# Optimization experiments

Hardware: AMD Instinct MI355X
Metric: run time of the kernel (lower is better)

The kernel has to match this reference:

```python
import jax, jax.numpy as jnp
import numpy as np

N_HEADS = 16
N_KV_HEADS = 4
HEAD_DIM = 128


def _rope(x, cos, sin):
    # x: [b, s, h, d]; cos/sin: [s, d//2]; interleaved pair rotation
    b, s, h, d = x.shape
    xp = x.reshape(b, s, h, d // 2, 2)
    x_r, x_i = xp[..., 0], xp[..., 1]
    c = cos[None, :, None, :]
    sn = sin[None, :, None, :]
    o_r = x_r * c - x_i * sn
    o_i = x_r * sn + x_i * c
    return jnp.stack([o_r, o_i], axis=-1).reshape(b, s, h, d)


def setup_inputs() -> dict:
    key = jax.random.key(0)
    ks = jax.random.split(key, 7)
    B, S, D = 2, 2048, 2048
    KV = N_KV_HEADS * HEAD_DIM
    x = jax.random.normal(ks[0], (B, S, D), dtype=jnp.float32)
    freqs_cos = jax.random.uniform(ks[1], (S, HEAD_DIM // 2), dtype=jnp.float32)
    freqs_sin = jax.random.uniform(ks[2], (S, HEAD_DIM // 2), dtype=jnp.float32)
    scale = 0.02
    wq = jax.random.normal(ks[3], (D, D), dtype=jnp.float32) * scale
    wk = jax.random.normal(ks[4], (KV, D), dtype=jnp.float32) * scale
    wv = jax.random.normal(ks[5], (KV, D), dtype=jnp.float32) * scale
    wo = jax.random.normal(ks[6], (D, D), dtype=jnp.float32) * scale
    return {"x": x, "freqs_cos": freqs_cos, "freqs_sin": freqs_sin,
            "wq": wq, "wk": wk, "wv": wv, "wo": wo}


def reference(x, freqs_cos, freqs_sin, wq, wk, wv, wo):
    B, S, D = x.shape
    n_rep = N_HEADS // N_KV_HEADS
    q = (x @ wq.T).reshape(B, S, N_HEADS, HEAD_DIM)
    k = (x @ wk.T).reshape(B, S, N_KV_HEADS, HEAD_DIM)
    v = (x @ wv.T).reshape(B, S, N_KV_HEADS, HEAD_DIM)
    q = _rope(q, freqs_cos, freqs_sin)
    k = _rope(k, freqs_cos, freqs_sin)
    # repeat_kv == torch.repeat_interleave along head dim
    k = jnp.repeat(k, n_rep, axis=2)
    v = jnp.repeat(v, n_rep, axis=2)
    q = q.transpose(0, 2, 1, 3)  # [B, H, S, d]
    k = k.transpose(0, 2, 1, 3)
    v = v.transpose(0, 2, 1, 3)
    scale = 1.0 / np.sqrt(HEAD_DIM).astype(np.float32)
    scores = jnp.einsum('bhqd,bhkd->bhqk', q, k) * scale
    causal = jnp.tril(jnp.ones((S, S), dtype=bool))
    scores = jnp.where(causal[None, None], scores, jnp.finfo(jnp.float32).min)
    probs = jax.nn.softmax(scores.astype(jnp.float32), axis=-1).astype(q.dtype)
    out = jnp.einsum('bhqk,bhkd->bhqd', probs, v)
    out = out.transpose(0, 2, 1, 3).reshape(B, S, N_HEADS * HEAD_DIM)
    return out @ wo.T
```

## Files before the change

### kernel.cpp

```cpp
#include <hip/hip_runtime.h>
#include <hip/hip_bf16.h>
#include <type_traits>

using bf16x8 = __attribute__((ext_vector_type(8))) short;
using f32x4  = __attribute__((ext_vector_type(4))) float;
using u16x8  = __attribute__((ext_vector_type(8))) unsigned short;
using u16x4  = __attribute__((ext_vector_type(4))) unsigned short;
using u32x4  = __attribute__((ext_vector_type(4))) unsigned int;

__device__ __forceinline__ float b2f(unsigned short u) {
    unsigned int x = ((unsigned int)u) << 16;
    return __builtin_bit_cast(float, x);
}
__device__ __forceinline__ unsigned short f2b(float f) {
    __hip_bfloat16 h = __float2bfloat16(f);
    return __builtin_bit_cast(unsigned short, h);
}

#if defined(__has_builtin)
#if __has_builtin(__builtin_amdgcn_exp2f)
#define EXP2F(x) __builtin_amdgcn_exp2f(x)
#else
#define EXP2F(x) exp2f(x)
#endif
#else
#define EXP2F(x) exp2f(x)
#endif

__device__ __forceinline__ void async_copy16(const void* g, void* l) {
    __builtin_amdgcn_global_load_lds(
        (const __attribute__((address_space(1))) unsigned int*)g,
        (__attribute__((address_space(3))) unsigned int*)l, 16, 0, 0);
}

#define MFMA16(a, b, c) __builtin_amdgcn_mfma_f32_16x16x32_bf16(a, b, c, 0, 0, 0)

#define BARRIER() do { asm volatile("" ::: "memory"); \
    __builtin_amdgcn_s_barrier(); asm volatile("" ::: "memory"); } while (0)
#define VMCNT6() asm volatile("s_waitcnt vmcnt(6)" ::: "memory")
#define VMCNT0() asm volatile("s_waitcnt vmcnt(0)" ::: "memory")

__global__ __launch_bounds__(256) void cvt_f32_to_bf16(
    const float* __restrict__ s, unsigned short* __restrict__ d, int n4)
{
    int i = blockIdx.x * blockDim.x + threadIdx.x;
    if (i >= n4) return;
    float4 v = ((const float4*)s)[i];
    ushort4 o;
    o.x = f2b(v.x); o.y = f2b(v.y); o.z = f2b(v.z); o.w = f2b(v.w);
    ((ushort4*)d)[i] = o;
}

__global__ __launch_bounds__(512, 2) void qkv_gemm(
    const unsigned short* __restrict__ A,
    const unsigned short* __restrict__ Wq,
    const unsigned short* __restrict__ Wk,
    const unsigned short* __restrict__ Wv,
    unsigned short* __restrict__ Q,
    unsigned short* __restrict__ Kk,
    unsigned short* __restrict__ V)
{
    const int K = 2048;
    __shared__ unsigned short ldsA[2][256 * 64];
    __shared__ unsigned short ldsB[2][256 * 64];

    int tid  = threadIdx.x;
    int w    = tid >> 6;
    int lane = tid & 63;
    int idx  = lane & 15;
    int quad = lane >> 4;
    int srow   = lane >> 3;
    int schunk = (lane & 7) ^ srow;

    int wfm = (w >> 2) * 64;
    int wfn = (w & 3) * 64;

    int bid = (blockIdx.x & 7) * 24 + (blockIdx.x >> 3);
    int bm = bid / 12;
    int bn = bid - bm * 12;
    int m0 = bm * 256;

    const unsigned short* Bt;
    unsigned short* C;
    int Nc, n0;
    if (bn < 8)       { Bt = Wq + (size_t)bn * 256 * K;        C = Q;  Nc = 2048; n0 = bn * 256; }
    else if (bn < 10) { Bt = Wk + (size_t)(bn - 8) * 256 * K;  C = Kk; Nc = 512;  n0 = (bn - 8) * 256; }
    else              { Bt = Wv + (size_t)(bn - 10) * 256 * K; C = V;  Nc = 512;  n0 = (bn - 10) * 256; }

    const unsigned short* Ab = A + (size_t)m0 * K;

    f32x4 acc[8][4];
    #pragma unroll
    for (int mf = 0; mf < 8; ++mf)
        #pragma unroll
        for (int nf = 0; nf < 4; ++nf) acc[mf][nf] = (f32x4){0.f, 0.f, 0.f, 0.f};

    bf16x8 a[4][2], b0[2][2], b1[2][2];

    auto STAGE = [&](const unsigned short* __restrict__ G, int rb, int kc,
                     unsigned short* dst) {
        #pragma unroll
        for (int i = 0; i < 2; ++i) {
            int R = (w * 2 + i) * 8;
            async_copy16(G + (size_t)(rb + R + srow) * K + kc + schunk * 8,
                         dst + (size_t)R * 64);
        }
    };
    auto LDA = [&](int d, int mh) {
        #pragma unroll
        for (int mi = 0; mi < 4; ++mi) {
            int r = mh * 128 + wfm + mi * 16 + idx;
            #pragma unroll
            for (int ks = 0; ks < 2; ++ks)
                a[mi][ks] = *(const bf16x8*)&ldsA[d][r * 64 + (((ks * 4 + quad) ^ (r & 7)) << 3)];
        }
    };
    auto LDB0 = [&](int d, int nh) {
        #pragma unroll
        for (int nj = 0; nj < 2; ++nj) {
            int r = wfn + nh * 32 + nj * 16 + idx;
            #pragma unroll
            for (int ks = 0; ks < 2; ++ks)
                b0[nj][ks] = *(const bf16x8*)&ldsB[d][r * 64 + (((ks * 4 + quad) ^ (r & 7)) << 3)];
        }
    };
    auto LDB1 = [&](int d, int nh) {
        #pragma unroll
        for (int nj = 0; nj < 2; ++nj) {
            int r = wfn + nh * 32 + nj * 16 + idx;
            #pragma unroll
            for (int ks = 0; ks < 2; ++ks)
                b1[nj][ks] = *(const bf16x8*)&ldsB[d][r * 64 + (((ks * 4 + quad) ^ (r & 7)) << 3)];
        }
    };
    auto MM0 = [&](int mh, int nh) {
        __builtin_amdgcn_s_setprio(1);
        #pragma unroll
        for (int mi = 0; mi < 4; ++mi)
            #pragma unroll
            for (int nj = 0; nj < 2; ++nj)
                #pragma unroll
                for (int ks = 0; ks < 2; ++ks)
                    acc[mh * 4 + mi][nh * 2 + nj] =
                        MFMA16(a[mi][ks], b0[nj][ks], acc[mh * 4 + mi][nh * 2 + nj]);
        __builtin_amdgcn_s_setprio(0);
    };
    auto MM1 = [&](int mh, int nh) {
        __builtin_amdgcn_s_setprio(1);
        #pragma unroll
        for (int mi = 0; mi < 4; ++mi)
            #pragma unroll
            for (int nj = 0; nj < 2; ++nj)
                #pragma unroll
                for (int ks = 0; ks < 2; ++ks)
                    acc[mh * 4 + mi][nh * 2 + nj] =
                        MFMA16(a[mi][ks], b1[nj][ks], acc[mh * 4 + mi][nh * 2 + nj]);
        __builtin_amdgcn_s_setprio(0);
    };

    STAGE(Ab, 0,   0,  &ldsA[0][0]);
    STAGE(Ab, 128, 0,  &ldsA[0][128 * 64]);
    STAGE(Bt, 0,   0,  &ldsB[0][0]);
    STAGE(Bt, 128, 0,  &ldsB[0][128 * 64]);
    STAGE(Ab, 0,   64, &ldsA[1][0]);
    STAGE(Bt, 0,   64, &ldsB[1][0]);
    STAGE(Bt, 128, 64, &ldsB[1][128 * 64]);
    VMCNT6();
    BARRIER();

    for (int it = 0; it < 15; ++it) {
        int u = 2 * it;
        LDA(0, 0); LDB0(0, 0);
        STAGE(Ab, 128, (u + 1) * 64, &ldsA[1][128 * 64]);
        BARRIER(); MM0(0, 0); BARRIER();
        LDB1(0, 1);
        STAGE(Ab, 0, (u + 2) * 64, &ldsA[0][0]);
        BARRIER(); MM1(0, 1); BARRIER();
        LDA(0, 1);
        STAGE(Bt, 0, (u + 2) * 64, &ldsB[0][0]);
        BARRIER(); MM1(1, 1); BARRIER();
        STAGE(Bt, 128, (u + 2) * 64, &ldsB[0][128 * 64]);
        VMCNT6();
        BARRIER(); MM0(1, 0); BARRIER();
        LDA(1, 0); LDB0(1, 0);
        STAGE(Ab, 128, (u + 2) * 64, &ldsA[0][128 * 64]);
        BARRIER(); MM0(0, 0); BARRIER();
        LDB1(1, 1);
        STAGE(Ab, 0, (u + 3) * 64, &ldsA[1][0]);
        BARRIER(); MM1(0, 1); BARRIER();
        LDA(1, 1);
        STAGE(Bt, 0, (u + 3) * 64, &ldsB[1][0]);
        BARRIER(); MM1(1, 1); BARRIER();
        STAGE(Bt, 128, (u + 3) * 64, &ldsB[1][128 * 64]);
        VMCNT6();
        BARRIER(); MM0(1, 0); BARRIER();
    }

    LDA(0, 0); LDB0(0, 0);
    STAGE(Ab, 128, 31 * 64, &ldsA[1][128 * 64]);
    BARRIER(); MM0(0, 0); BARRIER();
    LDB1(0, 1);
    BARRIER(); MM1(0, 1); BARRIER();
    LDA(0, 1);
    BARRIER(); MM1(1, 1); BARRIER();
    VMCNT0();
    BARRIER(); MM0(1, 0); BARRIER();
    LDA(1, 0); LDB0(1, 0);
    BARRIER(); MM0(0, 0); BARRIER();
    LDB1(1, 1);
    BARRIER(); MM1(0, 1); BARRIER();
    LDA(1, 1);
    BARRIER(); MM1(1, 1); BARRIER();
    MM0(1, 0);

    #pragma unroll
    for (int mf = 0; mf < 8; ++mf) {
        #pragma unroll
        for (int r = 0; r < 4; ++r) {
            size_t row = (size_t)(m0 + (mf >> 2) * 128 + wfm + (mf & 3) * 16 + quad * 4 + r);
            #pragma unroll
            for (int nf = 0; nf < 4; ++nf) {
                int col = n0 + wfn + nf * 16 + idx;
                C[row * Nc + col] = f2b(acc[mf][nf][r]);
            }
        }
    }
}

__device__ __forceinline__ void g_stage(
    const unsigned short* __restrict__ A, const unsigned short* __restrict__ Bt,
    unsigned short* As, unsigned short* Bs,
    int k0, int K, int w, int srow, int schunk)
{
    #pragma unroll
    for (int i = 0; i < 4; ++i) {
        int cb = w * 4 + i;
        size_t goff = (size_t)(cb * 8 + srow) * K + k0 + schunk * 8;
        async_copy16(A  + goff, &As[cb * 512]);
        async_copy16(Bt + goff, &Bs[cb * 512]);
    }
}
__device__ __forceinline__ void g_compute(
    const unsigned short* As, const unsigned short* Bs,
    f32x4 (&acc)[4][4], int wm, int wn, int idx, int quad)
{
    #pragma unroll
    for (int ks = 0; ks < 2; ++ks) {
        bf16x8 af[4], bfr[4];
        #pragma unroll
        for (int mi = 0; mi < 4; ++mi) {
            int row = wm + mi * 16 + idx;
            af[mi] = *(const bf16x8*)&As[row * 64 + (((ks * 4 + quad) ^ (row & 7)) * 8)];
        }
        #pragma unroll
        for (int ni = 0; ni < 4; ++ni) {
            int row = wn + ni * 16 + idx;
            bfr[ni] = *(const bf16x8*)&Bs[row * 64 + (((ks * 4 + quad) ^ (row & 7)) * 8)];
        }
        #pragma unroll
        for (int mi = 0; mi < 4; ++mi)
            #pragma unroll
            for (int ni = 0; ni < 4; ++ni)
                acc[mi][ni] = MFMA16(af[mi], bfr[ni], acc[mi][ni]);
    }
}

template <typename OutT>
__global__ __launch_bounds__(256) void gemm_tile(
    const unsigned short* __restrict__ A,
    const unsigned short* __restrict__ Bt,
    OutT* __restrict__ C,
    int M, int N, int K)
{
    constexpr int BK = 64;
    __shared__ unsigned short As0[128 * BK];
    __shared__ unsigned short Bs0[128 * BK];
    __shared__ unsigned short As1[128 * BK];
    __shared__ unsigned short Bs1[128 * BK];

    int tid  = threadIdx.x;
    int w    = tid >> 6;
    int lane = tid & 63;
    int idx  = lane & 15;
    int quad = lane >> 4;
    int wm   = (w >> 1) * 64;
    int wn   = (w & 1) * 64;

    int tilesN = N / 128;
    int bm = blockIdx.x / tilesN;
    int bn = blockIdx.x - bm * tilesN;
    int m0 = bm * 128, n0 = bn * 128;

    const unsigned short* Ab = A  + (size_t)m0 * K;
    const unsigned short* Bb = Bt + (size_t)n0 * K;

    int srow   = lane >> 3;
    int schunk = (lane & 7) ^ srow;

    f32x4 acc[4][4];
    #pragma unroll
    for (int mi = 0; mi < 4; ++mi)
        #pragma unroll
        for (int ni = 0; ni < 4; ++ni) acc[mi][ni] = (f32x4){0.f, 0.f, 0.f, 0.f};

    g_stage(Ab, Bb, As0, Bs0, 0, K, w, srow, schunk);
    __syncthreads();

    for (int k0 = 0; k0 < K; k0 += 2 * BK) {
        if (k0 + BK < K)
            g_stage(Ab, Bb, As1, Bs1, k0 + BK, K, w, srow, schunk);
        g_compute(As0, Bs0, acc, wm, wn, idx, quad);
        __syncthreads();
        if (k0 + 2 * BK < K)
            g_stage(Ab, Bb, As0, Bs0, k0 + 2 * BK, K, w, srow, schunk);
        g_compute(As1, Bs1, acc, wm, wn, idx, quad);
        __syncthreads();
    }

    #pragma unroll
    for (int mi = 0; mi < 4; ++mi) {
        #pragma unroll
        for (int r = 0; r < 4; ++r) {
            size_t row = (size_t)(m0 + wm + mi * 16 + quad * 4 + r);
            #pragma unroll
            for (int ni = 0; ni < 4; ++ni) {
                int col = n0 + wn + ni * 16 + idx;
                if constexpr (std::is_same_v<OutT, float>) {
                    C[row * N + col] = acc[mi][ni][r];
                } else {
                    C[row * N + col] = f2b(acc[mi][ni][r]);
                }
            }
        }
    }
}

__global__ __launch_bounds__(256) void rope_kernel(
    unsigned short* __restrict__ x,
    const float* __restrict__ cs,
    const float* __restrict__ sn,
    int H, int total, float oscale)
{
    int e = blockIdx.x * blockDim.x + threadIdx.x;
    if (e >= total) return;
    int i = e & 63;
    int s = (e / (64 * H)) & 2047;
    float xr = b2f(x[2 * e]);
    float xi = b2f(x[2 * e + 1]);
    float c  = cs[s * 64 + i];
    float sv = sn[s * 64 + i];
    x[2 * e]     = f2b((xr * c - xi * sv) * oscale);
    x[2 * e + 1] = f2b((xr * sv + xi * c) * oscale);
}

__global__ __launch_bounds__(256, 2) void flash_attn(
    const unsigned short* __restrict__ qg,
    const unsigned short* __restrict__ kk,
    const unsigned short* __restrict__ vv,
    unsigned short* __restrict__ out)
{
    const int S = 2048;
    int bid = blockIdx.x;
    int qp  = bid & 15;
    int bh  = bid >> 4;
    int h   = bh & 15;
    int b   = bh >> 4;
    int kvh = h >> 2;

    int p   = b ? (15 - qp) : qp;

    int tid  = threadIdx.x;
    int w    = tid >> 6;
    int lane = tid & 63;
    int idx  = lane & 15;
    int quad = lane >> 4;

    int qt  = 2 * p + (w >> 1);
    int wq0 = qt * 64 + (w & 1) * 32;
    int qrA = wq0 + idx;

    __shared__ unsigned short Ks[2][64 * 128];
    __shared__ unsigned short Vt[2][128 * 72];

    const unsigned short* kbase = kk + ((size_t)b * S * 4 + kvh) * 128;
    const unsigned short* vbase = vv + ((size_t)b * S * 4 + kvh) * 128;

    bf16x8 qfA[4], qfB[4];
    {
        const unsigned short* qa =
            qg + ((size_t)((b * S + wq0 + idx) * 16 + h)) * 128 + quad * 8;
        const unsigned short* qb2 =
            qg + ((size_t)((b * S + wq0 + 16 + idx) * 16 + h)) * 128 + quad * 8;
        #pragma unroll
        for (int ko = 0; ko < 4; ++ko) {
            qfA[ko] = *(const bf16x8*)(qa  + ko * 32);
            qfB[ko] = *(const bf16x8*)(qb2 + ko * 32);
        }
    }

    f32x4 accA[8], accB[8];
    #pragma unroll
    for (int n = 0; n < 8; ++n) {
        accA[n] = (f32x4){0.f, 0.f, 0.f, 0.f};
        accB[n] = (f32x4){0.f, 0.f, 0.f, 0.f};
    }
    float lsumA = 0.f, lsumB = 0.f;

    int dp = lane * 2;
    int swzslot = ((w ^ ((dp >> 3) & 3)) << 3);

    int nt = 2 * p + 2;

    unsigned int vld[2][8];

    auto STAGE_ISSUE = [&](int t, int d) {
        #pragma unroll
        for (int i = 0; i < 4; ++i) {
            int key = w * 16 + i * 4 + (lane >> 4);
            int sc  = (lane & 15) ^ (key & 7);
            async_copy16(kbase + ((size_t)(t * 64 + key)) * 512 + sc * 8,
                         &Ks[d][(w * 16 + i * 4) * 128]);
        }
        const unsigned short* vc = vbase + ((size_t)t * 64) * 512 + dp;
        #pragma unroll
        for (int hh = 0; hh < 2; ++hh)
            #pragma unroll
            for (int ii = 0; ii < 8; ++ii) {
                int gk = hh * 32 + w * 4 + (ii >> 1) + 16 * (ii & 1);
                vld[hh][ii] = *(const unsigned int*)(vc + (size_t)gk * 512);
            }
    };
    auto STAGE_WRITE = [&](int d) {
        #pragma unroll
        for (int hh = 0; hh < 2; ++hh) {
            u16x8 lo, hi;
            #pragma unroll
            for (int ii = 0; ii < 8; ++ii) {
                lo[ii] = (unsigned short)vld[hh][ii];
                hi[ii] = (unsigned short)(vld[hh][ii] >> 16);
            }
            *(u16x8*)&Vt[d][dp * 72 + hh * 32 + swzslot]       = lo;
            *(u16x8*)&Vt[d][(dp + 1) * 72 + hh * 32 + swzslot] = hi;
        }
    };

    STAGE_ISSUE(0, 0);
    VMCNT0();
    STAGE_WRITE(0);
    __syncthreads();

    for (int t = 0; t < nt; ++t) {
        int bc = t & 1;
        if (t + 1 < nt) STAGE_ISSUE(t + 1, bc ^ 1);

        if (t * 64 <= wq0 + 31) {
            f32x4 sA[4], sB[4];
            #pragma unroll
            for (int g = 0; g < 4; ++g) {
                sA[g] = (f32x4){0.f, 0.f, 0.f, 0.f};
                sB[g] = (f32x4){0.f, 0.f, 0.f, 0.f};
            }
            #pragma unroll
            for (int ko = 0; ko < 4; ++ko) {
                int ch = ((ko * 4 + quad) ^ (idx & 7)) * 8;
                #pragma unroll
                for (int g = 0; g < 4; ++g) {
                    bf16x8 kf = *(const bf16x8*)&Ks[bc][(g * 16 + idx) * 128 + ch];
                    sA[g] = MFMA16(kf, qfA[ko], sA[g]);
                    sB[g] = MFMA16(kf, qfB[ko], sB[g]);
                }
            }
            unsigned int pkA[2][4], pkB[2][4];
            if (t * 64 + 63 <= wq0) {
                #pragma unroll
                for (int hh = 0; hh < 2; ++hh)
                    #pragma unroll
                    for (int r = 0; r < 4; ++r) {
                        float a0 = EXP2F(sA[hh * 2][r]), a1 = EXP2F(sA[hh * 2 + 1][r]);
                        float b0_ = EXP2F(sB[hh * 2][r]), b1_ = EXP2F(sB[hh * 2 + 1][r]);
                        lsumA += a0 + a1;
                        lsumB += b0_ + b1_;
                        pkA[hh][r] = (unsigned int)f2b(a0) | ((unsigned int)f2b(a1) << 16);
                        pkB[hh][r] = (unsigned int)f2b(b0_) | ((unsigned int)f2b(b1_) << 16);
                    }
            } else {
                int LA = qrA - t * 64;
                int LB = LA + 16;
                #pragma unroll
                for (int hh = 0; hh < 2; ++hh)
                    #pragma unroll
                    for (int r = 0; r < 4; ++r) {
                        int kl = hh * 32 + quad * 4 + r;
                        float a0 = (kl      <= LA) ? EXP2F(sA[hh * 2][r]) : 0.f;
                        float a1 = (kl + 16 <= LA) ? EXP2F(sA[hh * 2 + 1][r]) : 0.f;
                        float b0_ = (kl      <= LB) ? EXP2F(sB[hh * 2][r]) : 0.f;
                        float b1_ = (kl + 16 <= LB) ? EXP2F(sB[hh * 2 + 1][r]) : 0.f;
                        lsumA += a0 + a1;
                        lsumB += b0_ + b1_;
                        pkA[hh][r] = (unsigned int)f2b(a0) | ((unsigned int)f2b(a1) << 16);
                        pkB[hh][r] = (unsigned int)f2b(b0_) | ((unsigned int)f2b(b1_) << 16);
                    }
            }
            u32x4 pA0 = {pkA[0][0], pkA[0][1], pkA[0][2], pkA[0][3]};
            u32x4 pA1 = {pkA[1][0], pkA[1][1], pkA[1][2], pkA[1][3]};
            u32x4 pB0 = {pkB[0][0], pkB[0][1], pkB[0][2], pkB[0][3]};
            u32x4 pB1 = {pkB[1][0], pkB[1][1], pkB[1][2], pkB[1][3]};
            bf16x8 pfA0 = __builtin_bit_cast(bf16x8, pA0);
            bf16x8 pfA1 = __builtin_bit_cast(bf16x8, pA1);
            bf16x8 pfB0 = __builtin_bit_cast(bf16x8, pB0);
            bf16x8 pfB1 = __builtin_bit_cast(bf16x8, pB1);
            #pragma unroll
            for (int n = 0; n < 8; ++n) {
                int rr = n * 16 + idx;
                int base = rr * 72 + ((quad ^ ((rr >> 3) & 3)) << 3);
                bf16x8 vf0 = *(const bf16x8*)&Vt[bc][base];
                bf16x8 vf1 = *(const bf16x8*)&Vt[bc][base + 32];
                accA[n] = MFMA16(vf0, pfA0, accA[n]);
                accA[n] = MFMA16(vf1, pfA1, accA[n]);
                accB[n] = MFMA16(vf0, pfB0, accB[n]);
                accB[n] = MFMA16(vf1, pfB1, accB[n]);
            }
        }

        if (t + 1 < nt) {
            VMCNT0();
            STAGE_WRITE(bc ^ 1);
        }
        __syncthreads();
    }

    lsumA += __shfl_xor(lsumA, 16);
    lsumA += __shfl_xor(lsumA, 32);
    lsumB += __shfl_xor(lsumB, 16);
    lsumB += __shfl_xor(lsumB, 32);
    float invA = 1.f / lsumA;
    float invB = 1.f / lsumB;
    size_t rowA = (size_t)(b * S + wq0 + idx) * 2048 + h * 128;
    size_t rowB = rowA + (size_t)16 * 2048;
    #pragma unroll
    for (int n = 0; n < 8; ++n) {
        ushort4 oA, oB;
        oA.x = f2b(accA[n][0] * invA);
        oA.y = f2b(accA[n][1] * invA);
        oA.z = f2b(accA[n][2] * invA);
        oA.w = f2b(accA[n][3] * invA);
        oB.x = f2b(accB[n][0] * invB);
        oB.y = f2b(accB[n][1] * invB);
        oB.z = f2b(accB[n][2] * invB);
        oB.w = f2b(accB[n][3] * invB);
        *(ushort4*)&out[rowA + n * 16 + quad * 4] = oA;
        *(ushort4*)&out[rowB + n * 16 + quad * 4] = oB;
    }
}

extern "C" void kernel_launch(void* const* d_in, const int* in_sizes, int n_in,
                              void* d_out, int out_size, void* d_ws, size_t ws_size,
                              hipStream_t stream)
{
    const float* x  = (const float*)d_in[0];
    const float* fc = (const float*)d_in[1];
    const float* fs = (const float*)d_in[2];
    const float* wq = (const float*)d_in[3];
    const float* wk = (const float*)d_in[4];
    const float* wv = (const float*)d_in[5];
    const float* wo = (const float*)d_in[6];
    float* out = (float*)d_out;

    const int B = 2, S = 2048, D = 2048, KV = 512;
    const int M = B * S;

    unsigned short* ws  = (unsigned short*)d_ws;
    unsigned short* xb  = ws;
    unsigned short* wqb = xb  + (size_t)M * D;
    unsigned short* wkb = wqb + (size_t)D * D;
    unsigned short* wvb = wkb + (size_t)KV * D;
    unsigned short* wob = wvb + (size_t)KV * D;
    unsigned short* qb  = wob + (size_t)D * D;
    unsigned short* kb  = qb  + (size_t)M * D;
    unsigned short* vb  = kb  + (size_t)M * KV;
    unsigned short* ao  = vb  + (size_t)M * KV;

    cvt_f32_to_bf16<<<dim3((M * D / 4) / 256), dim3(256), 0, stream>>>(x,  xb,  M * D / 4);
    cvt_f32_to_bf16<<<dim3((D * D / 4) / 256), dim3(256), 0, stream>>>(wq, wqb, D * D / 4);
    cvt_f32_to_bf16<<<dim3((KV * D / 4) / 256), dim3(256), 0, stream>>>(wk, wkb, KV * D / 4);
    cvt_f32_to_bf16<<<dim3((KV * D / 4) / 256), dim3(256), 0, stream>>>(wv, wvb, KV * D / 4);
    cvt_f32_to_bf16<<<dim3((D * D / 4) / 256), dim3(256), 0, stream>>>(wo, wob, D * D / 4);

    qkv_gemm<<<dim3(192), dim3(512), 0, stream>>>(xb, wqb, wkb, wvb, qb, kb, vb);

    int qpairs = B * S * 16 * 64;
    int kpairs = B * S * 4 * 64;
    const float c2 = 0.12752584f;
    rope_kernel<<<dim3(qpairs / 256), dim3(256), 0, stream>>>(qb, fc, fs, 16, qpairs, c2);
    rope_kernel<<<dim3(kpairs / 256), dim3(256), 0, stream>>>(kb, fc, fs, 4, kpairs, 1.0f);

    flash_attn<<<dim3(512), dim3(256), 0, stream>>>(qb, kb, vb, ao);

    gemm_tile<float><<<dim3((M / 128) * (D / 128)), dim3(256), 0, stream>>>(ao, wob, out, M, D, D);
}
```

Before: 312.9 us.

## Fuse RoPE into QKV GEMM epilogue and merge conversion kernels

The two RoPE kernels are removed and the rotation is applied in the QKV GEMM epilogue. Each lane fetches its pair partner's value with a lane xor shuffle and reads cos/sin from global memory, with the Q softmax scale folded in. The five fp32-to-bf16 conversion launches are merged into one kernel that picks its source buffer by index range. This saves a read/write pass over Q and K plus several launches, at the cost of extra global loads and shuffles in the GEMM epilogue.

Result: no change. 311.5 us (-0.4%).

```diff
diff --git a/kernel.cpp b/kernel.cpp
--- a/kernel.cpp
+++ b/kernel.cpp
@@ -40,15 +40,25 @@
 #define VMCNT6() asm volatile("s_waitcnt vmcnt(6)" ::: "memory")
 #define VMCNT0() asm volatile("s_waitcnt vmcnt(0)" ::: "memory")
 
-__global__ __launch_bounds__(256) void cvt_f32_to_bf16(
-    const float* __restrict__ s, unsigned short* __restrict__ d, int n4)
-{
-    int i = blockIdx.x * blockDim.x + threadIdx.x;
-    if (i >= n4) return;
-    float4 v = ((const float4*)s)[i];
+__global__ __launch_bounds__(256) void cvt_all(
+    const float* __restrict__ x,  const float* __restrict__ wq,
+    const float* __restrict__ wk, const float* __restrict__ wv,
+    const float* __restrict__ wo,
+    unsigned short* __restrict__ xb,  unsigned short* __restrict__ wqb,
+    unsigned short* __restrict__ wkb, unsigned short* __restrict__ wvb,
+    unsigned short* __restrict__ wob)
+{
+    int i = blockIdx.x * 256 + threadIdx.x;
+    const float* s; unsigned short* d; int j;
+    if (i < 2097152)      { s = x;  d = xb;  j = i; }
+    else if (i < 3145728) { s = wq; d = wqb; j = i - 2097152; }
+    else if (i < 3407872) { s = wk; d = wkb; j = i - 3145728; }
+    else if (i < 3670016) { s = wv; d = wvb; j = i - 3407872; }
+    else                  { s = wo; d = wob; j = i - 3670016; }
+    float4 v = ((const float4*)s)[j];
     ushort4 o;
     o.x = f2b(v.x); o.y = f2b(v.y); o.z = f2b(v.z); o.w = f2b(v.w);
-    ((ushort4*)d)[i] = o;
+    ((ushort4*)d)[j] = o;
 }
 
 __global__ __launch_bounds__(512, 2) void qkv_gemm(
@@ -56,6 +66,8 @@
     const unsigned short* __restrict__ Wq,
     const unsigned short* __restrict__ Wk,
     const unsigned short* __restrict__ Wv,
+    const float* __restrict__ fc,
+    const float* __restrict__ fs,
     unsigned short* __restrict__ Q,
     unsigned short* __restrict__ Kk,
     unsigned short* __restrict__ V)
@@ -213,15 +225,27 @@
     BARRIER(); MM1(1, 1); BARRIER();
     MM0(1, 0);
 
+    bool dorope = (bn < 10);
+    float osc = (bn < 8) ? 0.12752584f : 1.0f;
     #pragma unroll
     for (int mf = 0; mf < 8; ++mf) {
         #pragma unroll
         for (int r = 0; r < 4; ++r) {
             size_t row = (size_t)(m0 + (mf >> 2) * 128 + wfm + (mf & 3) * 16 + quad * 4 + r);
+            int srow_ = (int)(row & 2047) * 64;
             #pragma unroll
             for (int nf = 0; nf < 4; ++nf) {
                 int col = n0 + wfn + nf * 16 + idx;
-                C[row * Nc + col] = f2b(acc[mf][nf][r]);
+                float v = acc[mf][nf][r];
+                if (dorope) {
+                    float pv = __shfl_xor(v, 1);
+                    int fi = srow_ + ((col & 127) >> 1);
+                    float c  = fc[fi];
+                    float sv = fs[fi];
+                    v = (col & 1) ? (pv * sv + v * c) : (v * c - pv * sv);
+                    v *= osc;
+                }
+                C[row * Nc + col] = f2b(v);
             }
         }
     }
@@ -333,24 +357,6 @@
             }
         }
     }
-}
-
-__global__ __launch_bounds__(256) void rope_kernel(
-    unsigned short* __restrict__ x,
-    const float* __restrict__ cs,
-    const float* __restrict__ sn,
-    int H, int total, float oscale)
-{
-    int e = blockIdx.x * blockDim.x + threadIdx.x;
-    if (e >= total) return;
-    int i = e & 63;
-    int s = (e / (64 * H)) & 2047;
-    float xr = b2f(x[2 * e]);
-    float xi = b2f(x[2 * e + 1]);
-    float c  = cs[s * 64 + i];
-    float sv = sn[s * 64 + i];
-    x[2 * e]     = f2b((xr * c - xi * sv) * oscale);
-    x[2 * e + 1] = f2b((xr * sv + xi * c) * oscale);
 }
 
 __global__ __launch_bounds__(256, 2) void flash_attn(
@@ -580,19 +586,11 @@
     unsigned short* vb  = kb  + (size_t)M * KV;
     unsigned short* ao  = vb  + (size_t)M * KV;
 
-    cvt_f32_to_bf16<<<dim3((M * D / 4) / 256), dim3(256), 0, stream>>>(x,  xb,  M * D / 4);
-    cvt_f32_to_bf16<<<dim3((D * D / 4) / 256), dim3(256), 0, stream>>>(wq, wqb, D * D / 4);
-    cvt_f32_to_bf16<<<dim3((KV * D / 4) / 256), dim3(256), 0, stream>>>(wk, wkb, KV * D / 4);
-    cvt_f32_to_bf16<<<dim3((KV * D / 4) / 256), dim3(256), 0, stream>>>(wv, wvb, KV * D / 4);
-    cvt_f32_to_bf16<<<dim3((D * D / 4) / 256), dim3(256), 0, stream>>>(wo, wob, D * D / 4);
-
-    qkv_gemm<<<dim3(192), dim3(512), 0, stream>>>(xb, wqb, wkb, wvb, qb, kb, vb);
-
-    int qpairs = B * S * 16 * 64;
-    int kpairs = B * S * 4 * 64;
-    const float c2 = 0.12752584f;
-    rope_kernel<<<dim3(qpairs / 256), dim3(256), 0, stream>>>(qb, fc, fs, 16, qpairs, c2);
-    rope_kernel<<<dim3(kpairs / 256), dim3(256), 0, stream>>>(kb, fc, fs, 4, kpairs, 1.0f);
+    cvt_all<<<dim3(18432), dim3(256), 0, stream>>>(
+        x, wq, wk, wv, wo, xb, wqb, wkb, wvb, wob);
+
+    qkv_gemm<<<dim3(192), dim3(512), 0, stream>>>(
+        xb, wqb, wkb, wvb, fc, fs, qb, kb, vb);
 
     flash_attn<<<dim3(512), dim3(256), 0, stream>>>(qb, kb, vb, ao);
 
```
